# Kernel optimization log

Hardware: AMD Instinct MI355X
Metric: run time of the kernel (lower is better)

Reference implementation:

```python
import jax, jax.numpy as jnp
import numpy as np

G = 4        # split_group
H = 64       # hidden_size_t = 256 // 4 (causal -> //1)
I = 64       # input_size_t  = 256 // 4
EPS = 1e-5


def _lstm(x, W_ih, W_hh, b):
    """Grouped unidirectional LSTM, PyTorch gate order (i,f,g,o).
    x: (G,B,T,I); W_ih: (G,4H,I); W_hh: (G,4H,H); b: (G,4H) -> (G,B,T,H)"""
    g, bsz, t, _ = x.shape
    h_dim = W_hh.shape[-1]
    # precompute input projections for all timesteps
    xp = jnp.einsum('gbti,gki->gbtk', x, W_ih) + b[:, None, None, :]  # (G,B,T,4H)
    xp = jnp.moveaxis(xp, 2, 0)  # (T,G,B,4H)

    def step(carry, xt):
        h, c = carry
        gates = xt + jnp.einsum('gbh,gkh->gbk', h, W_hh)
        i_g, f_g, g_g, o_g = jnp.split(gates, 4, axis=-1)
        i_g = jax.nn.sigmoid(i_g)
        f_g = jax.nn.sigmoid(f_g)
        g_g = jnp.tanh(g_g)
        o_g = jax.nn.sigmoid(o_g)
        c = f_g * c + i_g * g_g
        h = o_g * jnp.tanh(c)
        return (h, c), h

    h0 = jnp.zeros((g, bsz, h_dim), x.dtype)
    _, hs = jax.lax.scan(step, (h0, h0), xp)  # hs: (T,G,B,H)
    return jnp.moveaxis(hs, 0, 2)  # (G,B,T,H)


def _bn(x, gamma, beta):
    """BatchNorm1d (training stats) over (B,T) per feature. x: (B,T,F)"""
    mean = x.mean(axis=(0, 1))
    var = x.var(axis=(0, 1))
    return (x - mean) * jax.lax.rsqrt(var + EPS) * gamma + beta


def setup_inputs() -> dict:
    key = jax.random.key(0)
    ks = jax.random.split(key, 12)
    s = 0.1
    F = G * H
    return {
        'inpt': jax.random.normal(ks[0], (32, 1000, 256), jnp.float32),
        'W_ih1': jax.random.normal(ks[1], (G, 4 * H, I), jnp.float32) * s,
        'W_hh1': jax.random.normal(ks[2], (G, 4 * H, H), jnp.float32) * s,
        'b1': jax.random.normal(ks[3], (G, 4 * H), jnp.float32) * s,
        'W_ih2': jax.random.normal(ks[4], (G, 4 * H, H), jnp.float32) * s,
        'W_hh2': jax.random.normal(ks[5], (G, 4 * H, H), jnp.float32) * s,
        'b2': jax.random.normal(ks[6], (G, 4 * H), jnp.float32) * s,
        'gamma1': jnp.ones((F,), jnp.float32) + jax.random.normal(ks[7], (F,)) * 0.01,
        'beta1': jax.random.normal(ks[8], (F,), jnp.float32) * 0.01,
        'gamma2': jnp.ones((F,), jnp.float32) + jax.random.normal(ks[9], (F,)) * 0.01,
        'beta2': jax.random.normal(ks[10], (F,), jnp.float32) * 0.01,
    }


def reference(inpt, W_ih1, W_hh1, b1, W_ih2, W_hh2, b2, gamma1, beta1, gamma2, beta2):
    B, T, F = inpt.shape
    # chunk along features -> (G,B,T,I)
    xg = jnp.transpose(inpt.reshape(B, T, G, I), (2, 0, 1, 3))
    y1 = _lstm(xg, W_ih1, W_hh1, b1)  # (G,B,T,H)
    # torch.stack(dim=-1) + flatten: feature index = h*G + g (interleaved)
    x = jnp.transpose(y1, (1, 2, 3, 0)).reshape(B, T, H * G)
    x = _bn(x, gamma1, beta1)
    # chunk again into G contiguous groups of size H
    xg2 = jnp.transpose(x.reshape(B, T, G, H), (2, 0, 1, 3))
    y2 = _lstm(xg2, W_ih2, W_hh2, b2)  # (G,B,T,H)
    # torch.cat(dim=-1): contiguous groups
    x = jnp.transpose(y2, (1, 2, 0, 3)).reshape(B, T, G * H)
    x = _bn(x, gamma2, beta2)
    return x
```

## Files before the change

### kernel.cpp

```cpp
#include <hip/hip_runtime.h>
#include <math.h>

#define G 4
#define H 64
#define T 1000
#define B 32
#define ROWS (B*T)
#define SS 8

typedef _Float16 f16;
typedef _Float16 f16x2 __attribute__((ext_vector_type(2)));

#if defined(__has_builtin)
#if __has_builtin(__builtin_amdgcn_fdot2)
#define HAVE_FDOT2 1
#endif
#endif

__device__ __forceinline__ float dot2(f16x2 a, f16x2 b, float c) {
#ifdef HAVE_FDOT2
    return __builtin_amdgcn_fdot2(a, b, c, false);
#else
    return fmaf((float)a[0], (float)b[0], fmaf((float)a[1], (float)b[1], c));
#endif
}

__device__ __forceinline__ float sigm(float x) {
    return 1.f / (1.f + __expf(-x));
}
__device__ __forceinline__ float tanh_f(float x) {
    return 2.f / (1.f + __expf(-2.f * x)) - 1.f;
}

typedef const __attribute__((address_space(1))) void gas_void;
typedef __attribute__((address_space(3))) void las_void;

template<int LAYER>
__device__ void rec_wave4(const float* __restrict__ xp,
                          const float* __restrict__ Whh,
                          float* __restrict__ out,
                          float* __restrict__ stateh, float* __restrict__ statec,
                          float* __restrict__ sums,
                          int t0, int t1, int tcmax)
{
    __builtin_amdgcn_s_setprio(1);
    __shared__ __align__(16) float xbuf[2][SS][4][256];
    __shared__ __align__(16) _Float16 hx[4][64];
    const int wv = threadIdx.x >> 6;
    const int c  = threadIdx.x & 63;
    const int sq = blockIdx.x * 4 + wv;
    const int g = sq >> 5, b = sq & 31;

    f16x2 wpk[4][32];
    #pragma unroll
    for (int gt = 0; gt < 4; ++gt) {
        const float2* wp = (const float2*)&Whh[(size_t)((g * 256 + gt * 64 + c) << 6)];
        #pragma unroll
        for (int k = 0; k < 32; ++k) {
            float2 v = wp[k];
            f16x2 r; r[0] = (f16)v.x; r[1] = (f16)v.y;
            wpk[gt][k] = r;
        }
    }

    f16x2 hpk[32];
    float cst;
    if (t0 == 0) {
        #pragma unroll
        for (int k = 0; k < 32; ++k) { f16x2 z; z[0] = (f16)0.f; z[1] = (f16)0.f; hpk[k] = z; }
        cst = 0.f;
    } else {
        const float2* sh = (const float2*)&stateh[sq * 64];
        #pragma unroll
        for (int k = 0; k < 32; ++k) {
            float2 v = sh[k];
            f16x2 r; r[0] = (f16)v.x; r[1] = (f16)v.y;
            hpk[k] = r;
        }
        cst = statec[sq * 64 + c];
    }

    const float* xpb = xp + (size_t)sq * tcmax * 256;

    #pragma unroll
    for (int j = 0; j < SS; ++j) {
        const float* gsrc = xpb + (size_t)j * 256 + c * 4;
        __builtin_amdgcn_global_load_lds((gas_void*)gsrc,
                                         (las_void*)&xbuf[0][j][wv][0], 16, 0, 0);
    }
    asm volatile("s_waitcnt vmcnt(0)" ::: "memory");
    __builtin_amdgcn_sched_barrier(0);

    float st_s = 0.f, st_ss = 0.f, hl = 0.f;
    const int ngrp = (t1 - t0) / SS;
    for (int grp = 0; grp < ngrp; ++grp) {
        const int cur = grp & 1;
        if (grp + 1 < ngrp) {
            const int lbase = (grp + 1) * SS;
            #pragma unroll
            for (int j = 0; j < SS; ++j) {
                const float* gsrc = xpb + (size_t)(lbase + j) * 256 + c * 4;
                __builtin_amdgcn_global_load_lds((gas_void*)gsrc,
                                                 (las_void*)&xbuf[cur ^ 1][j][wv][0],
                                                 16, 0, 0);
            }
        }
        #pragma unroll
        for (int j = 0; j < SS; ++j) {
            float pj0 = xbuf[cur][j][wv][c];
            float pj1 = xbuf[cur][j][wv][64 + c];
            float pj2 = xbuf[cur][j][wv][128 + c];
            float pj3 = xbuf[cur][j][wv][192 + c];
            float pre[4];
            {
                float a0 = 0.f, a1 = 0.f;
                #pragma unroll
                for (int k = 0; k < 32; k += 2) {
                    a0 = dot2(wpk[0][k],     hpk[k],     a0);
                    a1 = dot2(wpk[0][k + 1], hpk[k + 1], a1);
                }
                pre[0] = (a0 + a1) + pj0;
            }
            {
                float a0 = 0.f, a1 = 0.f;
                #pragma unroll
                for (int k = 0; k < 32; k += 2) {
                    a0 = dot2(wpk[1][k],     hpk[k],     a0);
                    a1 = dot2(wpk[1][k + 1], hpk[k + 1], a1);
                }
                pre[1] = (a0 + a1) + pj1;
            }
            {
                float a0 = 0.f, a1 = 0.f;
                #pragma unroll
                for (int k = 0; k < 32; k += 2) {
                    a0 = dot2(wpk[2][k],     hpk[k],     a0);
                    a1 = dot2(wpk[2][k + 1], hpk[k + 1], a1);
                }
                pre[2] = (a0 + a1) + pj2;
            }
            {
                float a0 = 0.f, a1 = 0.f;
                #pragma unroll
                for (int k = 0; k < 32; k += 2) {
                    a0 = dot2(wpk[3][k],     hpk[k],     a0);
                    a1 = dot2(wpk[3][k + 1], hpk[k + 1], a1);
                }
                pre[3] = (a0 + a1) + pj3;
            }
            float ig = sigm(pre[0]);
            float fg = sigm(pre[1]);
            float gg = tanh_f(pre[2]);
            float og = sigm(pre[3]);
            cst = fmaf(fg, cst, ig * gg);
            float h = og * tanh_f(cst);
            int t = t0 + grp * SS + j;
            if (LAYER == 1) out[((size_t)b * T + t) * 256 + c * 4 + g] = h;
            else            out[((size_t)b * T + t) * 256 + g * 64 + c] = h;
            st_s += h;
            st_ss = fmaf(h, h, st_ss);
            hl = h;
            hx[wv][c] = (f16)h;
            const float4* hp = (const float4*)&hx[wv][0];
            #pragma unroll
            for (int q = 0; q < 8; ++q) {
                float4 v = hp[q];
                hpk[q * 4 + 0] = __builtin_bit_cast(f16x2, v.x);
                hpk[q * 4 + 1] = __builtin_bit_cast(f16x2, v.y);
                hpk[q * 4 + 2] = __builtin_bit_cast(f16x2, v.z);
                hpk[q * 4 + 3] = __builtin_bit_cast(f16x2, v.w);
            }
        }
        asm volatile("s_waitcnt vmcnt(0)" ::: "memory");
        __builtin_amdgcn_sched_barrier(0);
    }
    stateh[sq * 64 + c] = hl;
    statec[sq * 64 + c] = cst;
    int f = (LAYER == 1) ? (c * 4 + g) : (g * 64 + c);
    atomicAdd(&sums[f], st_s);
    atomicAdd(&sums[256 + f], st_ss);
}

template<bool BN>
__device__ void proj_tile(int id,
                          const float* __restrict__ xin,
                          const float* __restrict__ Wih,
                          const float* __restrict__ bias,
                          const float* __restrict__ ac,
                          float* __restrict__ xp,
                          int t0, int tcn, int tcmax, int TT)
{
    __shared__ __align__(16) float xs[64][68];
    __shared__ __align__(16) float wsm[64][68];

    const int tt = id % TT; id /= TT;
    const int b = id & 31;
    const int g = id >> 5;
    const int tid = threadIdx.x;
    const int tx = tid & 15, ty = tid >> 4;

    #pragma unroll
    for (int j = 0; j < 4; ++j) {
        int idx = j * 1024 + tid * 4;
        int r = idx >> 6, ci = idx & 63;
        int tg = t0 + tt * 64 + r; if (tg > T - 1) tg = T - 1;
        float4 v = *(const float4*)&xin[((size_t)b * T + tg) * 256 + g * 64 + ci];
        if (BN) {
            float4 a4 = *(const float4*)&ac[g * 64 + ci];
            float4 c4 = *(const float4*)&ac[256 + g * 64 + ci];
            v.x = fmaf(v.x, a4.x, c4.x);
            v.y = fmaf(v.y, a4.y, c4.y);
            v.z = fmaf(v.z, a4.z, c4.z);
            v.w = fmaf(v.w, a4.w, c4.w);
        }
        *(float4*)&xs[r][ci] = v;
    }

    float* xpb = xp + (size_t)(g * 32 + b) * tcmax * 256;

    for (int kt = 0; kt < 4; ++kt) {
        __syncthreads();
        #pragma unroll
        for (int j = 0; j < 4; ++j) {
            int idx = j * 1024 + tid * 4;
            int r = idx >> 6, ci = idx & 63;
            float4 v = *(const float4*)&Wih[(size_t)((g * 256 + kt * 64 + r) << 6) + ci];
            *(float4*)&wsm[r][ci] = v;
        }
        __syncthreads();

        float acc[4][4] = {};
        #pragma unroll
        for (int i4 = 0; i4 < 16; ++i4) {
            float4 xv[4], wv[4];
            #pragma unroll
            for (int q = 0; q < 4; ++q) xv[q] = *(const float4*)&xs[ty * 4 + q][i4 * 4];
            #pragma unroll
            for (int q = 0; q < 4; ++q) wv[q] = *(const float4*)&wsm[tx + 16 * q][i4 * 4];
            #pragma unroll
            for (int a = 0; a < 4; ++a)
                #pragma unroll
                for (int q = 0; q < 4; ++q) {
                    acc[a][q] = fmaf(xv[a].x, wv[q].x, acc[a][q]);
                    acc[a][q] = fmaf(xv[a].y, wv[q].y, acc[a][q]);
                    acc[a][q] = fmaf(xv[a].z, wv[q].z, acc[a][q]);
                    acc[a][q] = fmaf(xv[a].w, wv[q].w, acc[a][q]);
                }
        }

        float bq[4];
        #pragma unroll
        for (int q = 0; q < 4; ++q) bq[q] = bias[g * 256 + kt * 64 + tx + 16 * q];
        #pragma unroll
        for (int a = 0; a < 4; ++a) {
            int tloc = tt * 64 + ty * 4 + a;
            if (tloc < tcn) {
                #pragma unroll
                for (int q = 0; q < 4; ++q)
                    xpb[(size_t)tloc * 256 + kt * 64 + tx + 16 * q] = acc[a][q] + bq[q];
            }
        }
    }
}

template<int LAYER, bool PBN>
__global__ __launch_bounds__(256, 1)
void fused3(const float* __restrict__ xpA, const float* __restrict__ Whh,
            float* __restrict__ out,
            float* __restrict__ stateh, float* __restrict__ statec,
            float* __restrict__ sums,
            int t0, int t1, int tcmax,
            const float* __restrict__ xin, const float* __restrict__ Wih,
            const float* __restrict__ bias, const float* __restrict__ acbn,
            float* __restrict__ xpB, int t0n, int tcnn, int TTn)
{
    if (blockIdx.x < 32) {
        rec_wave4<LAYER>(xpA, Whh, out, stateh, statec, sums, t0, t1, tcmax);
    } else {
        proj_tile<PBN>(blockIdx.x - 32, xin, Wih, bias, acbn, xpB,
                       t0n, tcnn, tcmax, TTn);
    }
}

template<bool BN>
__global__ __launch_bounds__(256)
void xp_proj(const float* __restrict__ xin, const float* __restrict__ Wih,
             const float* __restrict__ bias, const float* __restrict__ ac,
             float* __restrict__ xp, int t0, int tcn, int tcmax, int TT)
{
    proj_tile<BN>(blockIdx.x, xin, Wih, bias, ac, xp, t0, tcn, tcmax, TT);
}

template<int LAYER>
__global__ __launch_bounds__(256, 1)
void rec_kernel(const float* __restrict__ xin,
                const float* __restrict__ Wih,
                const float* __restrict__ Whh,
                const float* __restrict__ bias,
                const float* __restrict__ bnac,
                float* __restrict__ out)
{
    const int g = blockIdx.x & 3;
    const int b = blockIdx.x >> 2;
    const int k = threadIdx.x;

    __shared__ __align__(16) float xsh[2][64];
    __shared__ __align__(16) float hsh[64];
    __shared__ __align__(16) float gsh[256];

    float wih[64], whh[64];
    {
        const float4* wi = (const float4*)(Wih + (size_t)(g * 256 + k) * 64);
        const float4* wh = (const float4*)(Whh + (size_t)(g * 256 + k) * 64);
        #pragma unroll
        for (int i = 0; i < 16; ++i) {
            float4 v = wi[i];
            wih[4*i] = v.x; wih[4*i+1] = v.y; wih[4*i+2] = v.z; wih[4*i+3] = v.w;
            float4 u = wh[i];
            whh[4*i] = u.x; whh[4*i+1] = u.y; whh[4*i+2] = u.z; whh[4*i+3] = u.w;
        }
    }
    const float bk = bias[g * 256 + k];
    const long rowbase = (long)b * T;
    const int  colbase = g * 64;

    float c = 0.f, af = 1.f, cf = 0.f;
    float xa = 0.f, xb = 0.f;

    if (k < 64) {
        if (LAYER == 2) { af = bnac[colbase + k]; cf = bnac[256 + colbase + k]; }
        hsh[k] = 0.f;
        float x0 = xin[(rowbase + 0) * 256 + colbase + k];
        xsh[0][k] = (LAYER == 2) ? fmaf(x0, af, cf) : x0;
        xa = xin[(rowbase + 1) * 256 + colbase + k];
        xb = xin[(rowbase + 2) * 256 + colbase + k];
    }
    __syncthreads();

    for (int t = 0; t < T; ++t) {
        const int cur = t & 1;
        float xn = 0.f;
        if (k < 64) {
            int tp = t + 3; if (tp > T - 1) tp = T - 1;
            xn = xin[(rowbase + tp) * 256 + colbase + k];
        }
        const float* xs = xsh[cur];
        float a0 = 0.f, a1 = 0.f, a2 = 0.f, a3 = 0.f;
        #pragma unroll
        for (int i = 0; i < 64; i += 4) {
            a0 = fmaf(wih[i],     xs[i],     a0);
            a1 = fmaf(wih[i + 1], xs[i + 1], a1);
            a2 = fmaf(wih[i + 2], xs[i + 2], a2);
            a3 = fmaf(wih[i + 3], xs[i + 3], a3);
        }
        #pragma unroll
        for (int jq = 0; jq < 64; jq += 4) {
            a0 = fmaf(whh[jq],     hsh[jq],     a0);
            a1 = fmaf(whh[jq + 1], hsh[jq + 1], a1);
            a2 = fmaf(whh[jq + 2], hsh[jq + 2], a2);
            a3 = fmaf(whh[jq + 3], hsh[jq + 3], a3);
        }
        const float acc = bk + ((a0 + a1) + (a2 + a3));
        const float act = (k >= 128 && k < 192) ? tanh_f(acc) : sigm(acc);
        gsh[k] = act;
        __syncthreads();

        if (k < 64) {
            const float ig = gsh[k];
            const float fg = gsh[64 + k];
            const float gg = gsh[128 + k];
            const float og = gsh[192 + k];
            c = fmaf(fg, c, ig * gg);
            const float h = og * tanh_f(c);
            hsh[k] = h;
            const long rrow = rowbase + t;
            if (LAYER == 1) out[rrow * 256 + k * 4 + g] = h;
            else            out[rrow * 256 + colbase + k] = h;
            xsh[cur ^ 1][k] = fmaf(xa, af, cf);
            xa = xb; xb = xn;
        }
        __syncthreads();
    }
}

__global__ void zero_ws(float* sums, int n) {
    int i = blockIdx.x * blockDim.x + threadIdx.x;
    if (i < n) sums[i] = 0.f;
}

__global__ __launch_bounds__(256) void stats_reduce(const float* __restrict__ x,
                                                    float* __restrict__ sums)
{
    float s = 0.f, ss = 0.f;
    for (int r = blockIdx.x; r < ROWS; r += gridDim.x) {
        float v = x[(long)r * 256 + threadIdx.x];
        s += v;
        ss = fmaf(v, v, ss);
    }
    atomicAdd(&sums[threadIdx.x], s);
    atomicAdd(&sums[256 + threadIdx.x], ss);
}

__global__ void stats_finalize(const float* __restrict__ sums,
                               const float* __restrict__ gamma,
                               const float* __restrict__ beta,
                               float* __restrict__ ac)
{
    int f = threadIdx.x;
    const float invN = 1.f / (float)ROWS;
    float mean = sums[f] * invN;
    float var  = fmaf(-mean, mean, sums[256 + f] * invN);
    float a = gamma[f] * rsqrtf(var + 1e-5f);
    ac[f]       = a;
    ac[256 + f] = fmaf(-mean, a, beta[f]);
}

__global__ __launch_bounds__(256) void bn_apply(float* __restrict__ x,
                                                const float* __restrict__ ac)
{
    __shared__ float a_s[256], c_s[256];
    a_s[threadIdx.x] = ac[threadIdx.x];
    c_s[threadIdx.x] = ac[256 + threadIdx.x];
    __syncthreads();
    const long n4 = (long)ROWS * 64;
    for (long i = (long)blockIdx.x * blockDim.x + threadIdx.x; i < n4;
         i += (long)gridDim.x * blockDim.x) {
        float4 v = ((float4*)x)[i];
        int f0 = (int)((i * 4) & 255);
        v.x = fmaf(v.x, a_s[f0],     c_s[f0]);
        v.y = fmaf(v.y, a_s[f0 + 1], c_s[f0 + 1]);
        v.z = fmaf(v.z, a_s[f0 + 2], c_s[f0 + 2]);
        v.w = fmaf(v.w, a_s[f0 + 3], c_s[f0 + 3]);
        ((float4*)x)[i] = v;
    }
}

extern "C" void kernel_launch(void* const* d_in, const int* in_sizes, int n_in,
                              void* d_out, int out_size, void* d_ws, size_t ws_size,
                              hipStream_t stream)
{
    const float* inpt   = (const float*)d_in[0];
    const float* Wih1   = (const float*)d_in[1];
    const float* Whh1   = (const float*)d_in[2];
    const float* b1     = (const float*)d_in[3];
    const float* Wih2   = (const float*)d_in[4];
    const float* Whh2   = (const float*)d_in[5];
    const float* b2     = (const float*)d_in[6];
    const float* gamma1 = (const float*)d_in[7];
    const float* beta1  = (const float*)d_in[8];
    const float* gamma2 = (const float*)d_in[9];
    const float* beta2  = (const float*)d_in[10];
    float* out  = (float*)d_out;

    float* sums1 = (float*)d_ws;
    float* sums2 = sums1 + 512;
    float* acbn1 = sums2 + 512;
    float* acbn2 = acbn1 + 512;
    float* sth   = acbn2 + 512;
    float* stc   = sth + 8192;
    float* xpb   = stc + 8192;

    const size_t fixedB = (size_t)(4 * 512 + 2 * 8192) * 4;
    const long perT = 128L * 256L * 4L;
    long availPair = ((long)ws_size - (long)fixedB) / (2L * perT);

    int chunks[8]; int nch = 0;
    if (availPair >= 440) {
        chunks[0] = 128; chunks[1] = 440; chunks[2] = 432; nch = 3;
    } else if (availPair >= SS) {
        int Tc = (int)(availPair & ~(long)(SS - 1));
        int acc = 0;
        while (acc < T && nch < 8) {
            int c = T - acc; if (c > Tc) c = Tc;
            chunks[nch++] = c; acc += c;
        }
        if (acc < T) nch = 0;
    }

    if (nch > 0) {
        int tcmax = 0;
        for (int i = 0; i < nch; ++i) if (chunks[i] > tcmax) tcmax = chunks[i];
        float* buf[2] = { xpb, xpb + (size_t)tcmax * 128 * 256 };
        zero_ws<<<4, 256, 0, stream>>>(sums1, 1024);

        for (int layer = 1; layer <= 2; ++layer) {
            const float* xin  = (layer == 1) ? inpt : out;
            const float* Wih  = (layer == 1) ? Wih1 : Wih2;
            const float* Whh  = (layer == 1) ? Whh1 : Whh2;
            const float* bb   = (layer == 1) ? b1 : b2;
            float* sums       = (layer == 1) ? sums1 : sums2;

            int t0 = 0;
            int TT0 = (chunks[0] + 63) / 64;
            if (layer == 1)
                xp_proj<false><<<128 * TT0, 256, 0, stream>>>(
                    xin, Wih, bb, nullptr, buf[0], 0, chunks[0], tcmax, TT0);
            else
                xp_proj<true><<<128 * TT0, 256, 0, stream>>>(
                    xin, Wih, bb, acbn1, buf[0], 0, chunks[0], tcmax, TT0);

            for (int c = 0; c < nch; ++c) {
                int t1 = t0 + chunks[c];
                int t0n = t1;
                int tcnn = (c + 1 < nch) ? chunks[c + 1] : 0;
                int TTn = (tcnn + 63) / 64;
                int grid = 32 + 128 * TTn;
                if (layer == 1)
                    fused3<1, false><<<grid, 256, 0, stream>>>(
                        buf[c & 1], Whh, out, sth, stc, sums, t0, t1, tcmax,
                        xin, Wih, bb, nullptr, buf[(c + 1) & 1], t0n, tcnn, TTn);
                else
                    fused3<2, true><<<grid, 256, 0, stream>>>(
                        buf[c & 1], Whh, out, sth, stc, sums, t0, t1, tcmax,
                        xin, Wih, bb, acbn1, buf[(c + 1) & 1], t0n, tcnn, TTn);
                t0 = t1;
            }
            if (layer == 1)
                stats_finalize<<<1, 256, 0, stream>>>(sums1, gamma1, beta1, acbn1);
            else
                stats_finalize<<<1, 256, 0, stream>>>(sums2, gamma2, beta2, acbn2);
        }
        bn_apply<<<2048, 256, 0, stream>>>(out, acbn2);
    } else {
        zero_ws<<<2, 256, 0, stream>>>(sums1, 512);
        rec_kernel<1><<<G * B, 256, 0, stream>>>(inpt, Wih1, Whh1, b1, nullptr, out);
        stats_reduce<<<256, 256, 0, stream>>>(out, sums1);
        stats_finalize<<<1, 256, 0, stream>>>(sums1, gamma1, beta1, acbn1);
        rec_kernel<2><<<G * B, 256, 0, stream>>>(out, Wih2, Whh2, b2, acbn1, out);
        zero_ws<<<2, 256, 0, stream>>>(sums2, 512);
        stats_reduce<<<256, 256, 0, stream>>>(out, sums2);
        stats_finalize<<<1, 256, 0, stream>>>(sums2, gamma2, beta2, acbn2);
        bn_apply<<<2048, 256, 0, stream>>>(out, acbn2);
    }
}
```

Measured before the change: 1.379 ms.

## Run each LSTM sequence in its own single-wave block and shrink projection blocks

Each recurrent (g,b) sequence now gets its own 64-thread workgroup instead of packing four waves per 256-thread block, so the 128 sequences spread across more CUs and no longer share a CU's issue slots. The input-projection tile is reworked to run with 64 threads, each computing four row groups, so fused launches stay consistent with the 64-thread block size. The end-of-group wait is relaxed to vmcnt(8) so the next group's prefetch need not fully drain. The cost is more blocks competing for CUs and more per-thread work in the projection tiles; the relaxed wait is only safe if vmcnt counts the prefetch loads the way this assumes.

```diff
diff --git a/kernel.cpp b/kernel.cpp
--- a/kernel.cpp
+++ b/kernel.cpp
@@ -36,7 +36,7 @@
 typedef __attribute__((address_space(3))) void las_void;
 
 template<int LAYER>
-__device__ void rec_wave4(const float* __restrict__ xp,
+__device__ void rec_wave1(const float* __restrict__ xp,
                           const float* __restrict__ Whh,
                           float* __restrict__ out,
                           float* __restrict__ stateh, float* __restrict__ statec,
@@ -44,11 +44,10 @@
                           int t0, int t1, int tcmax)
 {
     __builtin_amdgcn_s_setprio(1);
-    __shared__ __align__(16) float xbuf[2][SS][4][256];
-    __shared__ __align__(16) _Float16 hx[4][64];
-    const int wv = threadIdx.x >> 6;
+    __shared__ __align__(16) float xbuf[2][SS][256];
+    __shared__ __align__(16) _Float16 hx[64];
     const int c  = threadIdx.x & 63;
-    const int sq = blockIdx.x * 4 + wv;
+    const int sq = blockIdx.x;
     const int g = sq >> 5, b = sq & 31;
 
     f16x2 wpk[4][32];
@@ -86,7 +85,7 @@
     for (int j = 0; j < SS; ++j) {
         const float* gsrc = xpb + (size_t)j * 256 + c * 4;
         __builtin_amdgcn_global_load_lds((gas_void*)gsrc,
-                                         (las_void*)&xbuf[0][j][wv][0], 16, 0, 0);
+                                         (las_void*)&xbuf[0][j][0], 16, 0, 0);
     }
     asm volatile("s_waitcnt vmcnt(0)" ::: "memory");
     __builtin_amdgcn_sched_barrier(0);
@@ -101,16 +100,16 @@
             for (int j = 0; j < SS; ++j) {
                 const float* gsrc = xpb + (size_t)(lbase + j) * 256 + c * 4;
                 __builtin_amdgcn_global_load_lds((gas_void*)gsrc,
-                                                 (las_void*)&xbuf[cur ^ 1][j][wv][0],
+                                                 (las_void*)&xbuf[cur ^ 1][j][0],
                                                  16, 0, 0);
             }
         }
         #pragma unroll
         for (int j = 0; j < SS; ++j) {
-            float pj0 = xbuf[cur][j][wv][c];
-            float pj1 = xbuf[cur][j][wv][64 + c];
-            float pj2 = xbuf[cur][j][wv][128 + c];
-            float pj3 = xbuf[cur][j][wv][192 + c];
+            float pj0 = xbuf[cur][j][c];
+            float pj1 = xbuf[cur][j][64 + c];
+            float pj2 = xbuf[cur][j][128 + c];
+            float pj3 = xbuf[cur][j][192 + c];
             float pre[4];
             {
                 float a0 = 0.f, a1 = 0.f;
@@ -160,8 +159,8 @@
             st_s += h;
             st_ss = fmaf(h, h, st_ss);
             hl = h;
-            hx[wv][c] = (f16)h;
-            const float4* hp = (const float4*)&hx[wv][0];
+            hx[c] = (f16)h;
+            const float4* hp = (const float4*)&hx[0];
             #pragma unroll
             for (int q = 0; q < 8; ++q) {
                 float4 v = hp[q];
@@ -171,7 +170,7 @@
                 hpk[q * 4 + 3] = __builtin_bit_cast(f16x2, v.w);
             }
         }
-        asm volatile("s_waitcnt vmcnt(0)" ::: "memory");
+        asm volatile("s_waitcnt vmcnt(8)" ::: "memory");
         __builtin_amdgcn_sched_barrier(0);
     }
     stateh[sq * 64 + c] = hl;
@@ -182,13 +181,13 @@
 }
 
 template<bool BN>
-__device__ void proj_tile(int id,
-                          const float* __restrict__ xin,
-                          const float* __restrict__ Wih,
-                          const float* __restrict__ bias,
-                          const float* __restrict__ ac,
-                          float* __restrict__ xp,
-                          int t0, int tcn, int tcmax, int TT)
+__device__ void proj_tile64(int id,
+                            const float* __restrict__ xin,
+                            const float* __restrict__ Wih,
+                            const float* __restrict__ bias,
+                            const float* __restrict__ ac,
+                            float* __restrict__ xp,
+                            int t0, int tcn, int tcmax, int TT)
 {
     __shared__ __align__(16) float xs[64][68];
     __shared__ __align__(16) float wsm[64][68];
@@ -200,8 +199,8 @@
     const int tx = tid & 15, ty = tid >> 4;
 
     #pragma unroll
-    for (int j = 0; j < 4; ++j) {
-        int idx = j * 1024 + tid * 4;
+    for (int j = 0; j < 16; ++j) {
+        int idx = j * 256 + tid * 4;
         int r = idx >> 6, ci = idx & 63;
         int tg = t0 + tt * 64 + r; if (tg > T - 1) tg = T - 1;
         float4 v = *(const float4*)&xin[((size_t)b * T + tg) * 256 + g * 64 + ci];
@@ -221,51 +220,55 @@
     for (int kt = 0; kt < 4; ++kt) {
         __syncthreads();
         #pragma unroll
-        for (int j = 0; j < 4; ++j) {
-            int idx = j * 1024 + tid * 4;
+        for (int j = 0; j < 16; ++j) {
+            int idx = j * 256 + tid * 4;
             int r = idx >> 6, ci = idx & 63;
             float4 v = *(const float4*)&Wih[(size_t)((g * 256 + kt * 64 + r) << 6) + ci];
             *(float4*)&wsm[r][ci] = v;
         }
         __syncthreads();
 
-        float acc[4][4] = {};
-        #pragma unroll
-        for (int i4 = 0; i4 < 16; ++i4) {
-            float4 xv[4], wv[4];
+        float bq[4];
+        #pragma unroll
+        for (int q = 0; q < 4; ++q) bq[q] = bias[g * 256 + kt * 64 + tx + 16 * q];
+
+        #pragma unroll
+        for (int rr = 0; rr < 4; ++rr) {
+            const int row0 = (rr * 4 + ty) * 4;
+            float acc[4][4] = {};
             #pragma unroll
-            for (int q = 0; q < 4; ++q) xv[q] = *(const float4*)&xs[ty * 4 + q][i4 * 4];
+            for (int i4 = 0; i4 < 16; ++i4) {
+                float4 xv[4], wv[4];
+                #pragma unroll
+                for (int q = 0; q < 4; ++q) xv[q] = *(const float4*)&xs[row0 + q][i4 * 4];
+                #pragma unroll
+                for (int q = 0; q < 4; ++q) wv[q] = *(const float4*)&wsm[tx + 16 * q][i4 * 4];
+                #pragma unroll
+                for (int a = 0; a < 4; ++a)
+                    #pragma unroll
+                    for (int q = 0; q < 4; ++q) {
+                        acc[a][q] = fmaf(xv[a].x, wv[q].x, acc[a][q]);
+                        acc[a][q] = fmaf(xv[a].y, wv[q].y, acc[a][q]);
+                        acc[a][q] = fmaf(xv[a].z, wv[q].z, acc[a][q]);
+                        acc[a][q] = fmaf(xv[a].w, wv[q].w, acc[a][q]);
+                    }
+            }
             #pragma unroll
-            for (int q = 0; q < 4; ++q) wv[q] = *(const float4*)&wsm[tx + 16 * q][i4 * 4];
-            #pragma unroll
-            for (int a = 0; a < 4; ++a)
-                #pragma unroll
-                for (int q = 0; q < 4; ++q) {
-                    acc[a][q] = fmaf(xv[a].x, wv[q].x, acc[a][q]);
-                    acc[a][q] = fmaf(xv[a].y, wv[q].y, acc[a][q]);
-                    acc[a][q] = fmaf(xv[a].z, wv[q].z, acc[a][q]);
-                    acc[a][q] = fmaf(xv[a].w, wv[q].w, acc[a][q]);
+            for (int a = 0; a < 4; ++a) {
+                int tloc = tt * 64 + row0 + a;
+                if (tloc < tcn) {
+                    #pragma unroll
+                    for (int q = 0; q < 4; ++q)
+                        xpb[(size_t)tloc * 256 + kt * 64 + tx + 16 * q] = acc[a][q] + bq[q];
                 }
-        }
-
-        float bq[4];
-        #pragma unroll
-        for (int q = 0; q < 4; ++q) bq[q] = bias[g * 256 + kt * 64 + tx + 16 * q];
-        #pragma unroll
-        for (int a = 0; a < 4; ++a) {
-            int tloc = tt * 64 + ty * 4 + a;
-            if (tloc < tcn) {
-                #pragma unroll
-                for (int q = 0; q < 4; ++q)
-                    xpb[(size_t)tloc * 256 + kt * 64 + tx + 16 * q] = acc[a][q] + bq[q];
             }
         }
     }
 }
 
 template<int LAYER, bool PBN>
-__global__ __launch_bounds__(256, 1)
-void fused3(const float* __restrict__ xpA, const float* __restrict__ Whh,
+__global__ __launch_bounds__(64, 1)
+void fused4(const float* __restrict__ xpA, const float* __restrict__ Whh,
             float* __restrict__ out,
             float* __restrict__ stateh, float* __restrict__ statec,
             float* __restrict__ sums,
@@ -274,21 +277,21 @@
             const float* __restrict__ bias, const float* __restrict__ acbn,
             float* __restrict__ xpB, int t0n, int tcnn, int TTn)
 {
-    if (blockIdx.x < 32) {
-        rec_wave4<LAYER>(xpA, Whh, out, stateh, statec, sums, t0, t1, tcmax);
+    if (blockIdx.x < 128) {
+        rec_wave1<LAYER>(xpA, Whh, out, stateh, statec, sums, t0, t1, tcmax);
     } else {
-        proj_tile<PBN>(blockIdx.x - 32, xin, Wih, bias, acbn, xpB,
-                       t0n, tcnn, tcmax, TTn);
+        proj_tile64<PBN>(blockIdx.x - 128, xin, Wih, bias, acbn, xpB,
+                         t0n, tcnn, tcmax, TTn);
     }
 }
 
 template<bool BN>
-__global__ __launch_bounds__(256)
-void xp_proj(const float* __restrict__ xin, const float* __restrict__ Wih,
-             const float* __restrict__ bias, const float* __restrict__ ac,
-             float* __restrict__ xp, int t0, int tcn, int tcmax, int TT)
-{
-    proj_tile<BN>(blockIdx.x, xin, Wih, bias, ac, xp, t0, tcn, tcmax, TT);
+__global__ __launch_bounds__(64)
+void xp_proj64(const float* __restrict__ xin, const float* __restrict__ Wih,
+               const float* __restrict__ bias, const float* __restrict__ ac,
+               float* __restrict__ xp, int t0, int tcn, int tcmax, int TT)
+{
+    proj_tile64<BN>(blockIdx.x, xin, Wih, bias, ac, xp, t0, tcn, tcmax, TT);
 }
 
 template<int LAYER>
@@ -493,10 +496,10 @@
             int t0 = 0;
             int TT0 = (chunks[0] + 63) / 64;
             if (layer == 1)
-                xp_proj<false><<<128 * TT0, 256, 0, stream>>>(
+                xp_proj64<false><<<128 * TT0, 64, 0, stream>>>(
                     xin, Wih, bb, nullptr, buf[0], 0, chunks[0], tcmax, TT0);
             else
-                xp_proj<true><<<128 * TT0, 256, 0, stream>>>(
+                xp_proj64<true><<<128 * TT0, 64, 0, stream>>>(
                     xin, Wih, bb, acbn1, buf[0], 0, chunks[0], tcmax, TT0);
 
             for (int c = 0; c < nch; ++c) {
@@ -504,13 +507,13 @@
                 int t0n = t1;
                 int tcnn = (c + 1 < nch) ? chunks[c + 1] : 0;
                 int TTn = (tcnn + 63) / 64;
-                int grid = 32 + 128 * TTn;
+                int grid = 128 + 128 * TTn;
                 if (layer == 1)
-                    fused3<1, false><<<grid, 256, 0, stream>>>(
+                    fused4<1, false><<<grid, 64, 0, stream>>>(
                         buf[c & 1], Whh, out, sth, stc, sums, t0, t1, tcmax,
                         xin, Wih, bb, nullptr, buf[(c + 1) & 1], t0n, tcnn, TTn);
                 else
-                    fused3<2, true><<<grid, 256, 0, stream>>>(
+                    fused4<2, true><<<grid, 64, 0, stream>>>(
                         buf[c & 1], Whh, out, sth, stc, sums, t0, t1, tcmax,
                         xin, Wih, bb, acbn1, buf[(c + 1) & 1], t0n, tcnn, TTn);
                 t0 = t1;
```

Measured after the change: 1.526 ms. 1.11x slower.
